# Kernel optimization log

Measured on AMD Instinct MI355X. Metric: run time of the kernel, lower is better.

Reference implementation:

```python
import jax, jax.numpy as jnp
import numpy as np

D = 1024; NH = 16; HD = 64; FF = 4096; DEPTH = 4
P = 14; C = 3; GRID = 32; MERGE = 2; NIMG = 4
L = GRID * GRID; S = NIMG * L; ORIG = 24; EPS = 1e-6
SCALE = HD ** -0.5


def setup_inputs() -> dict:
    key = jax.random.key(0)
    ks = jax.random.split(key, 12)
    s = 0.02
    return {
        "pixel_values": jax.random.normal(ks[0], (S, C * P * P), jnp.float32),
        "grid_thw": jnp.tile(jnp.array([[1, GRID, GRID]], jnp.int32), (NIMG, 1)),
        "conv_w": jax.random.normal(ks[1], (D, C * P * P), jnp.float32) * s,
        "conv_b": jnp.zeros((D,), jnp.float32),
        "pos_embed": jax.random.normal(ks[2], (ORIG * ORIG, D), jnp.float32) * s,
        "ln1_g": jnp.ones((DEPTH, D), jnp.float32),
        "ln1_b": jnp.zeros((DEPTH, D), jnp.float32),
        "qkv_w": jax.random.normal(ks[3], (DEPTH, 3 * D, D), jnp.float32) * s,
        "qkv_b": jnp.zeros((DEPTH, 3 * D), jnp.float32),
        "proj_w": jax.random.normal(ks[4], (DEPTH, D, D), jnp.float32) * s,
        "proj_b": jnp.zeros((DEPTH, D), jnp.float32),
        "ln2_g": jnp.ones((DEPTH, D), jnp.float32),
        "ln2_b": jnp.zeros((DEPTH, D), jnp.float32),
        "fc1_w": jax.random.normal(ks[5], (DEPTH, FF, D), jnp.float32) * s,
        "fc1_b": jnp.zeros((DEPTH, FF), jnp.float32),
        "fc2_w": jax.random.normal(ks[6], (DEPTH, D, FF), jnp.float32) * s,
        "fc2_b": jnp.zeros((DEPTH, D), jnp.float32),
    }


def _pos_ids():
    # rot_pos_emb spatial-merge permutation for one t=1 image, tiled over images
    h = jnp.broadcast_to(jnp.arange(GRID)[:, None], (GRID, GRID))
    w = jnp.broadcast_to(jnp.arange(GRID)[None, :], (GRID, GRID))
    def perm(a):
        a = a.reshape(GRID // MERGE, MERGE, GRID // MERGE, MERGE)
        return a.transpose(0, 2, 1, 3).reshape(-1)
    hpos = jnp.tile(perm(h), NIMG)  # [S]
    wpos = jnp.tile(perm(w), NIMG)
    return hpos, wpos


def _bilinear_border(img, nx, ny):
    # img [H, W, D]; nx, ny in [-1, 1]; align_corners=False, padding_mode='border'
    Hh, Ww, _ = img.shape
    x = (nx + 1.0) * 0.5 * Ww - 0.5
    y = (ny + 1.0) * 0.5 * Hh - 0.5
    x0 = jnp.floor(x); y0 = jnp.floor(y)
    wx = (x - x0)[:, None]; wy = (y - y0)[:, None]
    x0i = jnp.clip(x0.astype(jnp.int32), 0, Ww - 1)
    x1i = jnp.clip(x0.astype(jnp.int32) + 1, 0, Ww - 1)
    y0i = jnp.clip(y0.astype(jnp.int32), 0, Hh - 1)
    y1i = jnp.clip(y0.astype(jnp.int32) + 1, 0, Hh - 1)
    v00 = img[y0i, x0i]; v01 = img[y0i, x1i]
    v10 = img[y1i, x0i]; v11 = img[y1i, x1i]
    return (v00 * (1 - wy) * (1 - wx) + v01 * (1 - wy) * wx
            + v10 * wy * (1 - wx) + v11 * wy * wx)


def _ln(x, g, b):
    m = jnp.mean(x, axis=-1, keepdims=True)
    v = jnp.mean(jnp.square(x - m), axis=-1, keepdims=True)
    return (x - m) * jax.lax.rsqrt(v + EPS) * g + b


def _forward(pixel_values, conv_w, conv_b, pos_embed, ln1_g, ln1_b, qkv_w, qkv_b,
             proj_w, proj_b, ln2_g, ln2_b, fc1_w, fc1_b, fc2_w, fc2_b):
    # patch embed: conv with kernel==stride==patch over one patch == linear
    x = pixel_values @ conv_w.T + conv_b  # [S, D]

    # interpolated 2D position embedding (grid_sample bilinear, border pad)
    hpos, wpos = _pos_ids()
    norm_w = (wpos.astype(jnp.float32) + 0.5) / GRID * 2.0 - 1.0
    norm_h = (hpos.astype(jnp.float32) + 0.5) / GRID * 2.0 - 1.0
    pe = _bilinear_border(pos_embed.reshape(ORIG, ORIG, D), norm_w, norm_h)
    x = x + pe

    for i in range(DEPTH):
        # attention (block-diagonal over equal-length images -> batched)
        r = x
        y = _ln(x, ln1_g[i], ln1_b[i])
        qkv = (y @ qkv_w[i].T + qkv_b[i]).reshape(NIMG, L, 3, NH, HD)
        q = qkv[:, :, 0].transpose(0, 2, 1, 3)  # [B, H, L, hd]
        k = qkv[:, :, 1].transpose(0, 2, 1, 3)
        v = qkv[:, :, 2].transpose(0, 2, 1, 3)
        scores = jnp.einsum('bhqd,bhkd->bhqk', q, k) * SCALE
        probs = jax.nn.softmax(scores, axis=-1)
        o = jnp.einsum('bhqk,bhkd->bhqd', probs, v)
        o = o.transpose(0, 2, 1, 3).reshape(S, D)
        x = r + o @ proj_w[i].T + proj_b[i]
        # MLP
        r = x
        y = _ln(x, ln2_g[i], ln2_b[i])
        h = jax.nn.gelu(y @ fc1_w[i].T + fc1_b[i], approximate=False)
        x = r + h @ fc2_w[i].T + fc2_b[i]
    return x


def reference(pixel_values, grid_thw, conv_w, conv_b, pos_embed, ln1_g, ln1_b,
              qkv_w, qkv_b, proj_w, proj_b, ln2_g, ln2_b, fc1_w, fc1_b, fc2_w, fc2_b):
    return _forward(pixel_values, conv_w, conv_b, pos_embed, ln1_g, ln1_b, qkv_w,
                    qkv_b, proj_w, proj_b, ln2_g, ln2_b, fc1_w, fc1_b, fc2_w, fc2_b)
```

## Files before the change

kernel.cpp:

```cpp
#include <hip/hip_runtime.h>
#include <math.h>

typedef __bf16 bf16x8 __attribute__((ext_vector_type(8)));
typedef float f32x4 __attribute__((ext_vector_type(4)));
typedef short s16x4 __attribute__((ext_vector_type(4)));
typedef short s16x8 __attribute__((ext_vector_type(8)));

static __device__ __forceinline__ short f2bs(float f) {
  return __builtin_bit_cast(short, (__bf16)f);
}

#define GLL16(gp, lp) __builtin_amdgcn_global_load_lds( \
    (const __attribute__((address_space(1))) void*)(gp), \
    (__attribute__((address_space(3))) void*)(lp), 16, 0, 0)

__global__ __launch_bounds__(256) void cvt_f32_bf16(const float* __restrict__ s,
                                                    short* __restrict__ d, int n) {
  int stride = gridDim.x * blockDim.x * 4;
  for (int j = (blockIdx.x * blockDim.x + threadIdx.x) * 4; j < n; j += stride) {
    float4 v = *(const float4*)(s + j);
    s16x4 o;
    o[0] = f2bs(v.x); o[1] = f2bs(v.y); o[2] = f2bs(v.z); o[3] = f2bs(v.w);
    *(s16x4*)(d + j) = o;
  }
}

__global__ __launch_bounds__(256) void cvt_pad(const float* __restrict__ s,
                                               short* __restrict__ d) {
  int r = blockIdx.x;
  for (int c = threadIdx.x; c < 608; c += blockDim.x)
    d[(size_t)r * 608 + c] = (c < 588) ? f2bs(s[(size_t)r * 588 + c]) : (short)0;
}

template <int N, int K, int EPI, int CM, int CN>
__global__ __launch_bounds__(256) void gemm_bt(const short* __restrict__ A,
                                               const short* __restrict__ B,
                                               const float* __restrict__ bias,
                                               const float* __restrict__ resid,
                                               void* __restrict__ out) {
  static_assert(K % 32 == 0, "K");
  constexpr int NT = K / 32;
  static_assert(NT >= 3, "pipeline depth");
  constexpr int NX = N / 128, NY = 32;
  constexpr int nwg = NX * NY;
  static_assert(nwg % 8 == 0 && (nwg / 8) % (CM * CN) == 0, "chunk");
  static_assert(NX % CN == 0 && NY % CM == 0, "cells");
  __shared__ short lA[3][128 * 32];
  __shared__ short lB[3][128 * 32];

  const int o = blockIdx.x;
  const int wid = (o & 7) * (nwg / 8) + (o >> 3);
  constexpr int cellsz = CM * CN;
  const int cell = wid / cellsz, within = wid % cellsz;
  constexpr int cellsx = NX / CN;
  const int bm0 = ((cell / cellsx) * CM + within / CN) * 128;
  const int bn0 = ((cell % cellsx) * CN + within % CN) * 128;

  const int t = threadIdx.x, w = t >> 6, lane = t & 63;
  const int wr = w >> 1, wc = w & 1;
  f32x4 acc[4][4] = {};

  const int srow = t >> 2;
  const int scol = ((t & 3) ^ ((srow >> 1) & 3)) * 8;
  const short* aP = A + (size_t)(bm0 + srow) * K + scol;
  const short* bP = B + (size_t)(bn0 + srow) * K + scol;
  const int sdst0 = (w * 16) * 32;
  const int sdst1 = (64 + w * 16) * 32;

  const int lr = lane & 15;
  const int qx = ((lane >> 4) ^ ((lr >> 1) & 3)) * 8;

  auto stage = [&](int buf, int ko) {
    GLL16(aP + ko, &lA[buf][sdst0]);
    GLL16(aP + ko + (size_t)64 * K, &lA[buf][sdst1]);
    GLL16(bP + ko, &lB[buf][sdst0]);
    GLL16(bP + ko + (size_t)64 * K, &lB[buf][sdst1]);
  };

  stage(0, 0);
  stage(1, 32);
  stage(2, 64);

  int buf = 0;
  for (int kt = 0; kt < NT; ++kt) {
    if (kt < NT - 2)       asm volatile("s_waitcnt vmcnt(8)" ::: "memory");
    else if (kt == NT - 2) asm volatile("s_waitcnt vmcnt(4)" ::: "memory");
    else                   asm volatile("s_waitcnt vmcnt(0)" ::: "memory");
    __builtin_amdgcn_s_barrier();
    asm volatile("" ::: "memory");
    __builtin_amdgcn_sched_barrier(0);

    bf16x8 af[4], bg[4];
#pragma unroll
    for (int mi = 0; mi < 4; ++mi)
      af[mi] = *(const bf16x8*)&lA[buf][(wr * 64 + mi * 16 + lr) * 32 + qx];
#pragma unroll
    for (int ni = 0; ni < 4; ++ni)
      bg[ni] = *(const bf16x8*)&lB[buf][(wc * 64 + ni * 16 + lr) * 32 + qx];

    asm volatile("s_waitcnt lgkmcnt(0)" ::: "memory");
    __builtin_amdgcn_sched_barrier(0);
    __builtin_amdgcn_s_barrier();
    asm volatile("" ::: "memory");
    __builtin_amdgcn_sched_barrier(0);

    if (kt + 3 < NT) stage(buf, (kt + 3) * 32);
    __builtin_amdgcn_sched_barrier(0);

#pragma unroll
    for (int mi = 0; mi < 4; ++mi)
#pragma unroll
      for (int ni = 0; ni < 4; ++ni)
        acc[mi][ni] = __builtin_amdgcn_mfma_f32_16x16x32_bf16(af[mi], bg[ni],
                                                              acc[mi][ni], 0, 0, 0);
    buf = (buf == 2) ? 0 : buf + 1;
  }

  const int lg4 = (lane >> 4) * 4;
#pragma unroll
  for (int mi = 0; mi < 4; ++mi) {
#pragma unroll
    for (int ni = 0; ni < 4; ++ni) {
      const int row = bm0 + wr * 64 + mi * 16 + lg4;
      const int col = bn0 + wc * 64 + ni * 16 + lr;
      const float bc = bias[col];
#pragma unroll
      for (int r = 0; r < 4; ++r) {
        float v = acc[mi][ni][r] + bc;
        size_t idx = (size_t)(row + r) * N + col;
        if constexpr (EPI == 1) v = 0.5f * v * (1.0f + erff(v * 0.70710678118f));
        if constexpr (EPI == 0 || EPI == 1) ((short*)out)[idx] = f2bs(v);
        else if constexpr (EPI == 2) ((float*)out)[idx] = v + resid[idx];
        else ((float*)out)[idx] = v;
      }
    }
  }
}

template <int N, int K, int EPI, int CM, int CN>
__global__ __launch_bounds__(512, 2) void gemm256(const short* __restrict__ A,
                                                  const short* __restrict__ B,
                                                  const float* __restrict__ bias,
                                                  void* __restrict__ out) {
  static_assert(K % 64 == 0, "K");
  constexpr int NKT = K / 64;
  static_assert(NKT >= 3 && (NKT % 2) == 0, "ktiles");
  constexpr int NXT = N / 256, MYT = 16;
  constexpr int nwg = NXT * MYT;
  static_assert(nwg % 8 == 0 && (nwg / 8) % (CM * CN) == 0, "chunk");
  static_assert(NXT % CN == 0 && MYT % CM == 0, "cells");

  __shared__ short sA[2][2][8192];
  __shared__ short sB[2][2][8192];

  const int o = blockIdx.x;
  const int wid = (o & 7) * (nwg / 8) + (o >> 3);
  constexpr int cellsz = CM * CN;
  const int cell = wid / cellsz, within = wid % cellsz;
  constexpr int cellsx = NXT / CN;
  const int bm0 = ((cell / cellsx) * CM + within / CN) * 256;
  const int bn0 = ((cell % cellsx) * CN + within % CN) * 256;

  const int tid = threadIdx.x, wv = tid >> 6, lane = tid & 63;
  const int wrow = wv >> 2, wcol = wv & 3;
  const int lr = lane & 15, lg = lane >> 4;

  const int sr0 = tid >> 2;
  const int sc0 = ((tid & 3) ^ (sr0 & 3)) * 8;
  const short* aS0 = A + (size_t)(bm0 + sr0) * K + sc0;
  const short* bS0 = B + (size_t)(bn0 + sr0) * K + sc0;
  const int ld0 = wv * 512, ld1 = 4096 + wv * 512;

  auto stageA = [&](int d, int h, int kt) {
    const int off = kt * 64 + h * 32;
    GLL16(aS0 + off, &sA[d][h][ld0]);
    GLL16(aS0 + off + (size_t)128 * K, &sA[d][h][ld1]);
  };
  auto stageB = [&](int d, int h, int kt) {
    const int off = kt * 64 + h * 32;
    GLL16(bS0 + off, &sB[d][h][ld0]);
    GLL16(bS0 + off + (size_t)128 * K, &sB[d][h][ld1]);
  };

  const int chR = (lg ^ (lr & 3)) * 8;
  const int rA0 = wrow * 128 + lr;
  const int rB0 = wcol * 64 + lr;

  f32x4 acc[8][4] = {};

  stageA(0, 0, 0); stageB(0, 0, 0);
  stageA(0, 1, 0); stageB(0, 1, 0);
  stageA(1, 0, 1); stageB(1, 0, 1);
  asm volatile("s_waitcnt vmcnt(8)" ::: "memory");
  __builtin_amdgcn_sched_barrier(0);
  __builtin_amdgcn_s_barrier();

  bf16x8 af[4], bf[4];

#define LDA(mh, ks, d)                                                        \
  _Pragma("unroll")                                                           \
  for (int f = 0; f < 4; ++f)                                                 \
    af[f] = *(const bf16x8*)&sA[d][ks][(rA0 + (mh)*64 + f * 16) * 32 + chR];
#define LDB(ks, d)                                                            \
  _Pragma("unroll")                                                           \
  for (int n = 0; n < 4; ++n)                                                 \
    bf[n] = *(const bf16x8*)&sB[d][ks][(rB0 + n * 16) * 32 + chR];
#define MFMA16(mh)                                                            \
  __builtin_amdgcn_s_setprio(1);                                              \
  _Pragma("unroll")                                                           \
  for (int f = 0; f < 4; ++f)                                                 \
    _Pragma("unroll")                                                         \
    for (int n = 0; n < 4; ++n)                                               \
      acc[(mh)*4 + f][n] = __builtin_amdgcn_mfma_f32_16x16x32_bf16(           \
          af[f], bf[n], acc[(mh)*4 + f][n], 0, 0, 0);                         \
  __builtin_amdgcn_s_setprio(0);
#define PH_BAR1                                                               \
  __builtin_amdgcn_s_barrier();                                               \
  asm volatile("s_waitcnt lgkmcnt(0)" ::: "memory");                          \
  __builtin_amdgcn_sched_barrier(0);
#define PH_END                                                                \
  __builtin_amdgcn_s_barrier();
#define PH_END_V                                                              \
  asm volatile("s_waitcnt vmcnt(8)" ::: "memory");                            \
  __builtin_amdgcn_sched_barrier(0);                                          \
  __builtin_amdgcn_s_barrier();

  for (int t = 0; t < NKT; ++t) {
    const int d = t & 1;
    int t1 = t + 1; if (t1 >= NKT) t1 -= NKT;
    int t2 = t + 2; if (t2 >= NKT) t2 -= NKT;
    const int d1 = t1 & 1, d2 = t2 & 1;

    LDA(0, 0, d); LDB(0, d);
    stageA(d1, 1, t1);
    PH_BAR1; MFMA16(0); PH_END;
    LDA(1, 0, d);
    stageB(d1, 1, t1);
    PH_BAR1; MFMA16(1); PH_END_V;
    LDA(0, 1, d); LDB(1, d);
    stageA(d2, 0, t2);
    PH_BAR1; MFMA16(0); PH_END;
    LDA(1, 1, d);
    stageB(d2, 0, t2);
    PH_BAR1; MFMA16(1); PH_END_V;
  }
#undef LDA
#undef LDB
#undef MFMA16
#undef PH_BAR1
#undef PH_END
#undef PH_END_V

  const int lg4 = lg * 4;
#pragma unroll
  for (int mh = 0; mh < 2; ++mh) {
#pragma unroll
    for (int f = 0; f < 4; ++f) {
#pragma unroll
      for (int n = 0; n < 4; ++n) {
        const int row = bm0 + wrow * 128 + mh * 64 + f * 16 + lg4;
        const int col = bn0 + wcol * 64 + n * 16 + lr;
        const float bc = bias[col];
#pragma unroll
        for (int r = 0; r < 4; ++r) {
          float v = acc[mh * 4 + f][n][r] + bc;
          if constexpr (EPI == 1) v = 0.5f * v * (1.0f + erff(v * 0.70710678118f));
          ((short*)out)[(size_t)(row + r) * N + col] = f2bs(v);
        }
      }
    }
  }
}

__global__ __launch_bounds__(256) void ln_fwd(const float* __restrict__ x,
                                              const float* __restrict__ g,
                                              const float* __restrict__ b,
                                              short* __restrict__ y) {
  const int row = blockIdx.x, t = threadIdx.x, w = t >> 6, lane = t & 63;
  const float4 v = ((const float4*)(x + (size_t)row * 1024))[t];
  float s = v.x + v.y + v.z + v.w;
  float ss = v.x * v.x + v.y * v.y + v.z * v.z + v.w * v.w;
#pragma unroll
  for (int m = 1; m < 64; m <<= 1) { s += __shfl_xor(s, m); ss += __shfl_xor(ss, m); }
  __shared__ float rs[4], rss[4];
  if (lane == 0) { rs[w] = s; rss[w] = ss; }
  __syncthreads();
  s = rs[0] + rs[1] + rs[2] + rs[3];
  ss = rss[0] + rss[1] + rss[2] + rss[3];
  const float mean = s * (1.f / 1024.f);
  const float var = ss * (1.f / 1024.f) - mean * mean;
  const float rstd = rsqrtf(var + 1e-6f);
  const float4 gv = ((const float4*)g)[t];
  const float4 bv = ((const float4*)b)[t];
  s16x4 o;
  o[0] = f2bs((v.x - mean) * rstd * gv.x + bv.x);
  o[1] = f2bs((v.y - mean) * rstd * gv.y + bv.y);
  o[2] = f2bs((v.z - mean) * rstd * gv.z + bv.z);
  o[3] = f2bs((v.w - mean) * rstd * gv.w + bv.w);
  *(s16x4*)(y + (size_t)row * 1024 + t * 4) = o;
}

__global__ __launch_bounds__(256) void pos_add(float* __restrict__ x,
                                               const float* __restrict__ pe) {
  const int sidx = blockIdx.x;
  const int f = sidx & 1023;
  const int wq = 2 * ((f >> 2) & 15) + (f & 1);
  const int hq = 2 * (f >> 6) + ((f >> 1) & 1);
  const float gx = (wq + 0.5f) * 0.75f - 0.5f;
  const float gy = (hq + 0.5f) * 0.75f - 0.5f;
  const float fx = floorf(gx), fy = floorf(gy);
  const float wx = gx - fx, wy = gy - fy;
  int x0 = (int)fx, y0 = (int)fy;
  const int x0i = x0 < 0 ? 0 : (x0 > 23 ? 23 : x0);
  const int x1i = (x0 + 1) < 0 ? 0 : ((x0 + 1) > 23 ? 23 : x0 + 1);
  const int y0i = y0 < 0 ? 0 : (y0 > 23 ? 23 : y0);
  const int y1i = (y0 + 1) < 0 ? 0 : ((y0 + 1) > 23 ? 23 : y0 + 1);
  const float w00 = (1 - wy) * (1 - wx), w01 = (1 - wy) * wx;
  const float w10 = wy * (1 - wx), w11 = wy * wx;
  const int c = threadIdx.x * 4;
  const float4 p00 = *(const float4*)(pe + (size_t)(y0i * 24 + x0i) * 1024 + c);
  const float4 p01 = *(const float4*)(pe + (size_t)(y0i * 24 + x1i) * 1024 + c);
  const float4 p10 = *(const float4*)(pe + (size_t)(y1i * 24 + x0i) * 1024 + c);
  const float4 p11 = *(const float4*)(pe + (size_t)(y1i * 24 + x1i) * 1024 + c);
  float* xp = x + (size_t)sidx * 1024 + c;
  float4 xv = *(float4*)xp;
  xv.x += w00 * p00.x + w01 * p01.x + w10 * p10.x + w11 * p11.x;
  xv.y += w00 * p00.y + w01 * p01.y + w10 * p10.y + w11 * p11.y;
  xv.z += w00 * p00.z + w01 * p01.z + w10 * p10.z + w11 * p11.z;
  xv.w += w00 * p00.w + w01 * p01.w + w10 * p10.w + w11 * p11.w;
  *(float4*)xp = xv;
}

__global__ __launch_bounds__(256) void attn_fwd(const short* __restrict__ qkv,
                                                short* __restrict__ outp) {
  __shared__ short lK[2][64 * 64];
  __shared__ short Vt[2][64 * 72];
  const int t = threadIdx.x, w = t >> 6, lane = t & 63;
  const int b = blockIdx.y >> 4, h = blockIdx.y & 15;
  const int sbase = b * 1024;
  const int q0 = blockIdx.x * 64 + w * 16;
  const int lr = lane & 15, lg = lane >> 4;

  const short* qrow = qkv + (size_t)(sbase + q0 + lr) * 3072 + h * 64;
  const bf16x8 qf0 = *(const bf16x8*)(qrow + lg * 8);
  const bf16x8 qf1 = *(const bf16x8*)(qrow + 32 + lg * 8);

  const int krofs = t >> 3;
  const int kcol = ((t & 7) ^ (krofs & 7)) * 8;
  const short* ksrc = qkv + (size_t)(sbase + krofs) * 3072 + 1024 + h * 64 + kcol;
  const int vkv = t >> 2, vdp = t & 3;
  const short* vsrc = qkv + (size_t)(sbase + vkv) * 3072 + 2048 + h * 64 + vdp * 16;
  const int vph = vkv ^ (vdp << 4);

  f32x4 o[4] = {};
  float mrun = -1e30f, lsum = 0.f;

  s16x8 v0 = *(const s16x8*)vsrc;
  s16x8 v1 = *(const s16x8*)(vsrc + 8);
  GLL16(ksrc, &lK[0][(w * 8) * 64]);
  GLL16(ksrc + (size_t)32 * 3072, &lK[0][(32 + w * 8) * 64]);
#pragma unroll
  for (int j = 0; j < 8; ++j) Vt[0][(vdp * 16 + j) * 72 + vph] = v0[j];
#pragma unroll
  for (int j = 0; j < 8; ++j) Vt[0][(vdp * 16 + 8 + j) * 72 + vph] = v1[j];
  asm volatile("s_waitcnt vmcnt(0) lgkmcnt(0)" ::: "memory");
  __builtin_amdgcn_s_barrier();

  int buf = 0;
  for (int kb = 0; kb < 16; ++kb) {
    if (kb < 15) {
      const short* vs = vsrc + (size_t)(kb + 1) * 64 * 3072;
      v0 = *(const s16x8*)vs;
      v1 = *(const s16x8*)(vs + 8);
      const short* ks = ksrc + (size_t)(kb + 1) * 64 * 3072;
      GLL16(ks, &lK[buf ^ 1][(w * 8) * 64]);
      GLL16(ks + (size_t)32 * 3072, &lK[buf ^ 1][(32 + w * 8) * 64]);
    }

    f32x4 s[4];
    __builtin_amdgcn_s_setprio(1);
#pragma unroll
    for (int sub = 0; sub < 4; ++sub) {
      const int krow = (sub * 16 + lr) * 64;
      const bf16x8 kf0 = *(const bf16x8*)&lK[buf][krow + (lg ^ (lr & 7)) * 8];
      const bf16x8 kf1 = *(const bf16x8*)&lK[buf][krow + ((lg + 4) ^ (lr & 7)) * 8];
      f32x4 a = {};
      a = __builtin_amdgcn_mfma_f32_16x16x32_bf16(kf0, qf0, a, 0, 0, 0);
      a = __builtin_amdgcn_mfma_f32_16x16x32_bf16(kf1, qf1, a, 0, 0, 0);
      s[sub] = a;
    }
    __builtin_amdgcn_s_setprio(0);

    constexpr float SC = 0.125f * 1.44269504089f;
    float sl[16];
#pragma unroll
    for (int sub = 0; sub < 4; ++sub)
#pragma unroll
      for (int r = 0; r < 4; ++r) sl[sub * 4 + r] = s[sub][r] * SC;
    float tm = sl[0];
#pragma unroll
    for (int i = 1; i < 16; ++i) tm = fmaxf(tm, sl[i]);
    tm = fmaxf(tm, __shfl_xor(tm, 16));
    tm = fmaxf(tm, __shfl_xor(tm, 32));
    if (!__all(tm <= mrun + 12.0f)) {
      const float newm = fmaxf(mrun, tm);
      const float sc = exp2f(mrun - newm);
      lsum *= sc;
#pragma unroll
      for (int f = 0; f < 4; ++f) {
        o[f][0] *= sc; o[f][1] *= sc; o[f][2] *= sc; o[f][3] *= sc;
      }
      mrun = newm;
    }
    s16x4 pb[4];
    float psum = 0.f;
#pragma unroll
    for (int sub = 0; sub < 4; ++sub)
#pragma unroll
      for (int r = 0; r < 4; ++r) {
        const float p = exp2f(sl[sub * 4 + r] - mrun);
        psum += p;
        pb[sub][r] = f2bs(p);
      }
    psum += __shfl_xor(psum, 16);
    psum += __shfl_xor(psum, 32);
    lsum += psum;

    __builtin_amdgcn_s_setprio(1);
#pragma unroll
    for (int f = 0; f < 4; ++f) {
      const int vrow = (f * 16 + lr) * 72;
#pragma unroll
      for (int sub = 0; sub < 4; ++sub) {
        const s16x4 va = *(const s16x4*)&Vt[buf][vrow + ((sub ^ f) << 4) + lg * 4];
        o[f] = __builtin_amdgcn_mfma_f32_16x16x16bf16_1k(va, pb[sub], o[f], 0, 0, 0);
      }
    }
    __builtin_amdgcn_s_setprio(0);

    if (kb < 15) {
#pragma unroll
      for (int j = 0; j < 8; ++j) Vt[buf ^ 1][(vdp * 16 + j) * 72 + vph] = v0[j];
#pragma unroll
      for (int j = 0; j < 8; ++j) Vt[buf ^ 1][(vdp * 16 + 8 + j) * 72 + vph] = v1[j];
      asm volatile("s_waitcnt vmcnt(0) lgkmcnt(0)" ::: "memory");
      __builtin_amdgcn_s_barrier();
      buf ^= 1;
    }
  }

  const float inv = 1.0f / lsum;
  short* orow = outp + (size_t)(sbase + q0 + lr) * 1024 + h * 64;
#pragma unroll
  for (int f = 0; f < 4; ++f) {
    s16x4 ov;
    ov[0] = f2bs(o[f][0] * inv); ov[1] = f2bs(o[f][1] * inv);
    ov[2] = f2bs(o[f][2] * inv); ov[3] = f2bs(o[f][3] * inv);
    *(s16x4*)(orow + f * 16 + lg * 4) = ov;
  }
}

extern "C" void kernel_launch(void* const* d_in, const int* in_sizes, int n_in,
                              void* d_out, int out_size, void* d_ws, size_t ws_size,
                              hipStream_t stream) {
  const float* pixel  = (const float*)d_in[0];
  const float* conv_w = (const float*)d_in[2];
  const float* conv_b = (const float*)d_in[3];
  const float* pos_e  = (const float*)d_in[4];
  const float* ln1_g  = (const float*)d_in[5];
  const float* ln1_b  = (const float*)d_in[6];
  const float* qkv_w  = (const float*)d_in[7];
  const float* qkv_b  = (const float*)d_in[8];
  const float* proj_w = (const float*)d_in[9];
  const float* proj_b = (const float*)d_in[10];
  const float* ln2_g  = (const float*)d_in[11];
  const float* ln2_b  = (const float*)d_in[12];
  const float* fc1_w  = (const float*)d_in[13];
  const float* fc1_b  = (const float*)d_in[14];
  const float* fc2_w  = (const float*)d_in[15];
  const float* fc2_b  = (const float*)d_in[16];

  char* ws = (char*)d_ws;
  short* wQKV  = (short*)(ws + 0);
  short* wPROJ = (short*)(ws + 25165824);
  short* wFC1  = (short*)(ws + 33554432);
  short* wFC2  = (short*)(ws + 67108864);
  float* X     = (float*)(ws + 100663296);
  short* Y     = (short*)(ws + 117440512);
  short* QKVB  = (short*)(ws + 125829120);
  short* ATTNO = (short*)(ws + 150994944);
  short* H     = QKVB;
  short* WPIX  = QKVB;
  short* WCONV = (short*)(ws + 125829120 + 4980736);

  cvt_f32_bf16<<<2048, 256, 0, stream>>>(qkv_w, wQKV, 4 * 3072 * 1024);
  cvt_f32_bf16<<<1024, 256, 0, stream>>>(proj_w, wPROJ, 4 * 1024 * 1024);
  cvt_f32_bf16<<<2048, 256, 0, stream>>>(fc1_w, wFC1, 4 * 4096 * 1024);
  cvt_f32_bf16<<<2048, 256, 0, stream>>>(fc2_w, wFC2, 4 * 1024 * 4096);
  cvt_pad<<<4096, 256, 0, stream>>>(pixel, WPIX);
  cvt_pad<<<1024, 256, 0, stream>>>(conv_w, WCONV);

  gemm_bt<1024, 608, 3, 4, 8><<<256, 256, 0, stream>>>(WPIX, WCONV, conv_b, nullptr, X);
  pos_add<<<4096, 256, 0, stream>>>(X, pos_e);

  for (int i = 0; i < 4; ++i) {
    ln_fwd<<<4096, 256, 0, stream>>>(X, ln1_g + i * 1024, ln1_b + i * 1024, Y);
    gemm256<3072, 1024, 0, 8, 3><<<192, 512, 0, stream>>>(
        Y, wQKV + (size_t)i * 3072 * 1024, qkv_b + i * 3072, QKVB);
    attn_fwd<<<dim3(16, 64), 256, 0, stream>>>(QKVB, ATTNO);
    gemm_bt<1024, 1024, 2, 4, 8><<<256, 256, 0, stream>>>(
        ATTNO, wPROJ + (size_t)i * 1024 * 1024, proj_b + i * 1024, X, X);
    ln_fwd<<<4096, 256, 0, stream>>>(X, ln2_g + i * 1024, ln2_b + i * 1024, Y);
    gemm256<4096, 1024, 1, 8, 4><<<256, 512, 0, stream>>>(
        Y, wFC1 + (size_t)i * 4096 * 1024, fc1_b + i * 4096, H);
    float* dest = (i < 3) ? X : (float*)d_out;
    gemm_bt<1024, 4096, 2, 4, 8><<<256, 256, 0, stream>>>(
        H, wFC2 + (size_t)i * 1024 * 4096, fc2_b + i * 1024, X, dest);
  }
}
```

Before: 1.063 ms.

## Split-K the FC2 GEMM onto the 256x256 kernel with a fused reduce

Adds a split-K mode to the 256x256 GEMM kernel, with a K chunk, leading dimension and split count. FC2 (N=1024, K=4096) now runs as four K-chunks that write fp32 partials to workspace. A separate reduce kernel sums the partials and adds bias and residual. The LDS swizzle pattern also changes from row&3 to (row>>1)&3, presumably to cut bank conflicts. The goal is to fill the GPU with larger tiles for the narrow-N FC2 GEMM, at the cost of 64MB of partial writes and reads plus an extra launch. It falls back to the old path when the workspace is too small.

```diff
diff --git a/kernel.cpp b/kernel.cpp
--- a/kernel.cpp
+++ b/kernel.cpp
@@ -137,17 +137,19 @@
   }
 }
 
-template <int N, int K, int EPI, int CM, int CN>
+template <int N, int KC, int LDK, int EPI, int CM, int CN, int KSPLIT>
 __global__ __launch_bounds__(512, 2) void gemm256(const short* __restrict__ A,
                                                   const short* __restrict__ B,
                                                   const float* __restrict__ bias,
                                                   void* __restrict__ out) {
-  static_assert(K % 64 == 0, "K");
-  constexpr int NKT = K / 64;
+  static_assert(KC % 64 == 0, "K");
+  constexpr int NKT = KC / 64;
   static_assert(NKT >= 3 && (NKT % 2) == 0, "ktiles");
   constexpr int NXT = N / 256, MYT = 16;
-  constexpr int nwg = NXT * MYT;
-  static_assert(nwg % 8 == 0 && (nwg / 8) % (CM * CN) == 0, "chunk");
+  constexpr int nwg = NXT * MYT * KSPLIT;
+  constexpr int cellsz = CM * CN;
+  static_assert(nwg % 8 == 0 && (nwg / 8) % cellsz == 0, "chunk");
+  static_assert((NXT * MYT) % cellsz == 0, "cellspace");
   static_assert(NXT % CN == 0 && MYT % CM == 0, "cells");
 
   __shared__ short sA[2][2][8192];
@@ -155,8 +157,9 @@
 
   const int o = blockIdx.x;
   const int wid = (o & 7) * (nwg / 8) + (o >> 3);
-  constexpr int cellsz = CM * CN;
-  const int cell = wid / cellsz, within = wid % cellsz;
+  const int kc = wid / (NXT * MYT);
+  const int rem = wid % (NXT * MYT);
+  const int cell = rem / cellsz, within = rem % cellsz;
   constexpr int cellsx = NXT / CN;
   const int bm0 = ((cell / cellsx) * CM + within / CN) * 256;
   const int bn0 = ((cell % cellsx) * CN + within % CN) * 256;
@@ -166,23 +169,23 @@
   const int lr = lane & 15, lg = lane >> 4;
 
   const int sr0 = tid >> 2;
-  const int sc0 = ((tid & 3) ^ (sr0 & 3)) * 8;
-  const short* aS0 = A + (size_t)(bm0 + sr0) * K + sc0;
-  const short* bS0 = B + (size_t)(bn0 + sr0) * K + sc0;
+  const int sc0 = ((tid & 3) ^ ((sr0 >> 1) & 3)) * 8;
+  const short* aS0 = A + (size_t)(bm0 + sr0) * LDK + kc * KC + sc0;
+  const short* bS0 = B + (size_t)(bn0 + sr0) * LDK + kc * KC + sc0;
   const int ld0 = wv * 512, ld1 = 4096 + wv * 512;
 
   auto stageA = [&](int d, int h, int kt) {
     const int off = kt * 64 + h * 32;
     GLL16(aS0 + off, &sA[d][h][ld0]);
-    GLL16(aS0 + off + (size_t)128 * K, &sA[d][h][ld1]);
+    GLL16(aS0 + off + (size_t)128 * LDK, &sA[d][h][ld1]);
   };
   auto stageB = [&](int d, int h, int kt) {
     const int off = kt * 64 + h * 32;
     GLL16(bS0 + off, &sB[d][h][ld0]);
-    GLL16(bS0 + off + (size_t)128 * K, &sB[d][h][ld1]);
+    GLL16(bS0 + off + (size_t)128 * LDK, &sB[d][h][ld1]);
   };
 
-  const int chR = (lg ^ (lr & 3)) * 8;
+  const int chR = (lg ^ ((lr >> 1) & 3)) * 8;
   const int rA0 = wrow * 128 + lr;
   const int rB0 = wcol * 64 + lr;
 
@@ -260,16 +263,39 @@
       for (int n = 0; n < 4; ++n) {
         const int row = bm0 + wrow * 128 + mh * 64 + f * 16 + lg4;
         const int col = bn0 + wcol * 64 + n * 16 + lr;
-        const float bc = bias[col];
+        float bc = 0.f;
+        if constexpr (EPI != 5) bc = bias[col];
 #pragma unroll
         for (int r = 0; r < 4; ++r) {
           float v = acc[mh * 4 + f][n][r] + bc;
           if constexpr (EPI == 1) v = 0.5f * v * (1.0f + erff(v * 0.70710678118f));
-          ((short*)out)[(size_t)(row + r) * N + col] = f2bs(v);
+          if constexpr (EPI == 5)
+            ((float*)out)[((size_t)kc << 22) + (size_t)(row + r) * N + col] = v;
+          else
+            ((short*)out)[(size_t)(row + r) * N + col] = f2bs(v);
         }
       }
     }
   }
+}
+
+__global__ __launch_bounds__(256) void fc2_reduce(const float* __restrict__ part,
+                                                  const float* __restrict__ bias,
+                                                  const float* __restrict__ resid,
+                                                  float* __restrict__ dest) {
+  const size_t i4 = ((size_t)blockIdx.x * 256 + threadIdx.x) * 4;
+  const float4 a0 = *(const float4*)(part + i4);
+  const float4 a1 = *(const float4*)(part + (1ull << 22) + i4);
+  const float4 a2 = *(const float4*)(part + (2ull << 22) + i4);
+  const float4 a3 = *(const float4*)(part + (3ull << 22) + i4);
+  const float4 rv = *(const float4*)(resid + i4);
+  const float4 bv = *(const float4*)(bias + (i4 & 1023));
+  float4 o;
+  o.x = a0.x + a1.x + a2.x + a3.x + rv.x + bv.x;
+  o.y = a0.y + a1.y + a2.y + a3.y + rv.y + bv.y;
+  o.z = a0.z + a1.z + a2.z + a3.z + rv.z + bv.z;
+  o.w = a0.w + a1.w + a2.w + a3.w + rv.w + bv.w;
+  *(float4*)(dest + i4) = o;
 }
 
 __global__ __launch_bounds__(256) void ln_fwd(const float* __restrict__ x,
@@ -492,6 +518,8 @@
   short* H     = QKVB;
   short* WPIX  = QKVB;
   short* WCONV = (short*)(ws + 125829120 + 4980736);
+  float* PART  = (float*)(ws + 159383552);
+  const bool wsbig = ws_size >= (size_t)159383552 + 67108864;
 
   cvt_f32_bf16<<<2048, 256, 0, stream>>>(qkv_w, wQKV, 4 * 3072 * 1024);
   cvt_f32_bf16<<<1024, 256, 0, stream>>>(proj_w, wPROJ, 4 * 1024 * 1024);
@@ -505,16 +533,22 @@
 
   for (int i = 0; i < 4; ++i) {
     ln_fwd<<<4096, 256, 0, stream>>>(X, ln1_g + i * 1024, ln1_b + i * 1024, Y);
-    gemm256<3072, 1024, 0, 8, 3><<<192, 512, 0, stream>>>(
+    gemm256<3072, 1024, 1024, 0, 8, 3, 1><<<192, 512, 0, stream>>>(
         Y, wQKV + (size_t)i * 3072 * 1024, qkv_b + i * 3072, QKVB);
     attn_fwd<<<dim3(16, 64), 256, 0, stream>>>(QKVB, ATTNO);
     gemm_bt<1024, 1024, 2, 4, 8><<<256, 256, 0, stream>>>(
         ATTNO, wPROJ + (size_t)i * 1024 * 1024, proj_b + i * 1024, X, X);
     ln_fwd<<<4096, 256, 0, stream>>>(X, ln2_g + i * 1024, ln2_b + i * 1024, Y);
-    gemm256<4096, 1024, 1, 8, 4><<<256, 512, 0, stream>>>(
+    gemm256<4096, 1024, 1024, 1, 8, 4, 1><<<256, 512, 0, stream>>>(
         Y, wFC1 + (size_t)i * 4096 * 1024, fc1_b + i * 4096, H);
     float* dest = (i < 3) ? X : (float*)d_out;
-    gemm_bt<1024, 4096, 2, 4, 8><<<256, 256, 0, stream>>>(
-        H, wFC2 + (size_t)i * 1024 * 4096, fc2_b + i * 1024, X, dest);
-  }
-}
+    if (wsbig) {
+      gemm256<1024, 1024, 4096, 5, 8, 4, 4><<<256, 512, 0, stream>>>(
+          H, wFC2 + (size_t)i * 1024 * 4096, nullptr, PART);
+      fc2_reduce<<<4096, 256, 0, stream>>>(PART, fc2_b + i * 1024, X, dest);
+    } else {
+      gemm_bt<1024, 4096, 2, 4, 8><<<256, 256, 0, stream>>>(
+          H, wFC2 + (size_t)i * 1024 * 4096, fc2_b + i * 1024, X, dest);
+    }
+  }
+}
```

Result: faster. 1.022 ms (-3.8%).
